# Performance work log

Measured on AMD Instinct MI355X. Metric: run time of the kernel, lower is better.

The kernel has to match this reference:

```python
import jax, jax.numpy as jnp
import numpy as np

B, N, H, FE, M, PASSES, OUT = 512, 40, 128, 16, 128, 3, 128
NEG = -1e9


def setup_inputs() -> dict:
    key = jax.random.key(0)
    ks = jax.random.split(key, 16)
    am = jax.random.bernoulli(ks[0], 0.1, (B, N, N))
    am = (am | jnp.swapaxes(am, 1, 2)) & (~jnp.eye(N, dtype=bool))[None]
    edges = jax.random.uniform(ks[1], (B, N, N, FE), dtype=jnp.float32) * am[..., None].astype(jnp.float32)
    nodes = jax.random.normal(ks[2], (B, N, H), dtype=jnp.float32)
    s = lambda f: 1.0 / np.sqrt(f)
    return {
        "nodes": nodes,
        "edges": edges,
        "We": jax.random.normal(ks[3], (FE, M), dtype=jnp.float32) * s(FE),
        "Wn": jax.random.normal(ks[4], (H, M), dtype=jnp.float32) * s(H),
        "Wm": jax.random.normal(ks[5], (H, M), dtype=jnp.float32) * s(H),
        "Wi": jax.random.normal(ks[6], (M, 3 * H), dtype=jnp.float32) * s(M),
        "Wh": jax.random.normal(ks[7], (H, 3 * H), dtype=jnp.float32) * s(H),
        "bi": jnp.zeros((3 * H,), jnp.float32),
        "bh": jnp.zeros((3 * H,), jnp.float32),
        "Wg": jax.random.normal(ks[8], (2 * H, OUT), dtype=jnp.float32) * s(2 * H),
        "bg": jnp.zeros((OUT,), jnp.float32),
        "Wo": jax.random.normal(ks[9], (2 * H, OUT), dtype=jnp.float32) * s(2 * H),
        "bo": jnp.zeros((OUT,), jnp.float32),
    }


def _forward(nodes, edges, We, Wn, Wm, Wi, Wh, bi, bh, Wg, bg, Wo, bo):
    adj = jnp.sum(edges, axis=3)                      # (B,N,N)
    nghb_mask = adj > 0                               # neighbor exists
    node_mask = jnp.any(nghb_mask, axis=-1)           # (B,N) node has >=1 neighbor

    h = nodes                                         # hidden == input feature dim
    edge_proj = jnp.einsum("bijf,fm->bijm", edges, We)  # precompute, edges fixed
    for _ in range(PASSES):
        # attention energies over neighbors j of node i (masked softmax)
        nghb_proj = jnp.einsum("bjh,hm->bjm", h, Wn)  # (B,N,M)
        e = jnp.tanh(edge_proj + nghb_proj[:, None, :, :])        # (B,N,N,M)
        e = jnp.where(nghb_mask[..., None], e, NEG)
        att = jax.nn.softmax(e, axis=2)                            # over neighbor axis j
        emb = jnp.einsum("bjh,hm->bjm", h, Wm)                     # (B,N,M)
        messages = jnp.einsum("bijm,bjm->bim", att, emb)           # (B,N,M)
        # GRU cell update (only for existing nodes, as in the node-batch scatter)
        gi = messages @ Wi + bi
        gh = h @ Wh + bh
        r = jax.nn.sigmoid(gi[..., :H] + gh[..., :H])
        z = jax.nn.sigmoid(gi[..., H:2 * H] + gh[..., H:2 * H])
        n = jnp.tanh(gi[..., 2 * H:] + r * gh[..., 2 * H:])
        h_new = (1.0 - z) * n + z * h
        h = jnp.where(node_mask[..., None], h_new, h)

    # gated graph readout over existing nodes
    cat = jnp.concatenate([h, nodes], axis=-1)        # (B,N,2H)
    gate = jax.nn.sigmoid(cat @ Wg + bg)
    emb_out = cat @ Wo + bo
    out = jnp.sum(node_mask[..., None] * gate * emb_out, axis=1)   # (B,OUT)
    return out


def reference(nodes, edges, We, Wn, Wm, Wi, Wh, bi, bh, Wg, bg, Wo, bo):
    return _forward(nodes, edges, We, Wn, Wm, Wi, Wh, bi, bh, Wg, bg, Wo, bo)
```

## Files before the change

### kernel.cpp

```cpp
#include <hip/hip_runtime.h>

#define T 512
constexpr int Bc = 512, Nc = 40, Hc = 128, FEc = 16, Mc = 128, OUTc = 128, NPASS = 3;
constexpr int ROWP = 136;
constexpr int NPP  = 132;
constexpr int EPOOL = 512;

typedef __attribute__((ext_vector_type(8))) short short8;
typedef __attribute__((ext_vector_type(4))) float floatx4;
typedef __attribute__((ext_vector_type(4))) float fvec4;
typedef _Float16 half2v __attribute__((ext_vector_type(2)));
typedef _Float16 half8v __attribute__((ext_vector_type(8)));

constexpr int WS_WN = 0, WS_WM = 16384, WS_WI = 32768, WS_WH = 81920, WS_WG = 131072, WS_WO = 163840;

__device__ __forceinline__ float fast_rcp(float x) { return __builtin_amdgcn_rcpf(x); }
__device__ __forceinline__ float fast_sigmoid(float x) { return fast_rcp(1.f + __expf(-x)); }
__device__ __forceinline__ float fast_tanh(float x) {
    float t = __expf(2.f * x);
    return 1.f - 2.f * fast_rcp(t + 1.f);
}
__device__ __forceinline__ float bf2f(unsigned short u) {
    union { unsigned int i; float f; } v; v.i = ((unsigned int)u) << 16; return v.f;
}
__device__ __forceinline__ unsigned short f2bf(float f) {
    union { float f; unsigned int i; } v; v.f = f;
    unsigned int r = v.i + 0x7fff + ((v.i >> 16) & 1);
    return (unsigned short)(r >> 16);
}
__device__ __forceinline__ half2v u2h(unsigned int u) {
    union { unsigned int i; half2v h; } v; v.i = u; return v.h;
}

__device__ __forceinline__ floatx4 mm(short8 a, short8 b, floatx4 c) {
    return __builtin_amdgcn_mfma_f32_16x16x32_bf16(a, b, c, 0, 0, 0);
}
__device__ __forceinline__ short8 afrag(const unsigned short* buf, int mt, int kt, int lane) {
    int row = mt * 16 + (lane & 15); row = row > 39 ? 39 : row;
    return *(const short8*)(buf + row * ROWP + kt * 32 + (lane >> 4) * 8);
}
__device__ __forceinline__ short8 bfrag(const unsigned short* w, int nt, int nKT, int kt, int lane) {
    return *(const short8*)(w + ((nt * nKT + kt) * 64 + lane) * 8);
}

__global__ void prep_kernel(const float* __restrict__ Wn, const float* __restrict__ Wm,
                            const float* __restrict__ Wi, const float* __restrict__ Wh,
                            const float* __restrict__ Wg, const float* __restrict__ Wo,
                            unsigned short* __restrict__ ws) {
    int c = blockIdx.x, lane = threadIdx.x;
    int quad = lane >> 4, l16 = lane & 15;
    const float* W; int N, nKT, local; unsigned short* dst;
    if (c < 32)       { W = Wn; N = 128; nKT = 4; local = c;       dst = ws + WS_WN; }
    else if (c < 64)  { W = Wm; N = 128; nKT = 4; local = c - 32;  dst = ws + WS_WM; }
    else if (c < 160) { W = Wi; N = 384; nKT = 4; local = c - 64;  dst = ws + WS_WI; }
    else if (c < 256) { W = Wh; N = 384; nKT = 4; local = c - 160; dst = ws + WS_WH; }
    else if (c < 320) { W = Wg; N = 128; nKT = 8; local = c - 256; dst = ws + WS_WG; }
    else              { W = Wo; N = 128; nKT = 8; local = c - 320; dst = ws + WS_WO; }
    int nt = local / nKT, kt = local % nKT;
    short8 v;
#pragma unroll
    for (int j = 0; j < 8; ++j) {
        int k = kt * 32 + quad * 8 + j;
        v[j] = (short)f2bf(W[k * N + nt * 16 + l16]);
    }
    *(short8*)(dst + local * 512 + lane * 8) = v;
}

__global__ __launch_bounds__(T, 4) void mpnn_kernel(
    const float* __restrict__ nodes, const float* __restrict__ edges,
    const float* __restrict__ We, const float* __restrict__ bi,
    const float* __restrict__ bh, const float* __restrict__ bg,
    const float* __restrict__ bo, const unsigned short* __restrict__ ws,
    float* __restrict__ out)
{
    __shared__ __attribute__((aligned(16))) unsigned short s_hb[Nc * ROWP];
    __shared__ __attribute__((aligned(16))) unsigned short s_mb[Nc * ROWP];
    __shared__ __attribute__((aligned(16))) float s_np[Nc * NPP];
    __shared__ __attribute__((aligned(16))) unsigned short s_eb[Nc * ROWP];
    __shared__ __attribute__((aligned(16))) _Float16 s_poolh[EPOOL * FEc];
    __shared__ unsigned char s_nbr[Nc][Nc];
    __shared__ int s_cnt[Nc];
    __shared__ int s_off[Nc];
    __shared__ int s_total;

    const int b = blockIdx.x, tid = threadIdx.x;
    const int lane = tid & 63, wave = tid >> 6;
    const int quad = lane >> 4, l16 = lane & 15;
    const int m = tid & 127, g = tid >> 7;
    const int col = wave * 16 + l16;

    const float* nodes_b = nodes + (size_t)b * Nc * Hc;
    const float* edges_b = edges + (size_t)b * Nc * Nc * FEc;
    const unsigned short* wWn = ws + WS_WN; const unsigned short* wWm = ws + WS_WM;
    const unsigned short* wWi = ws + WS_WI; const unsigned short* wWh = ws + WS_WH;
    const unsigned short* wWg = ws + WS_WG; const unsigned short* wWo = ws + WS_WO;

    float hreg[3][4];
#pragma unroll
    for (int mt = 0; mt < 3; ++mt)
#pragma unroll
        for (int reg = 0; reg < 4; ++reg) {
            int row = mt * 16 + quad * 4 + reg;
            float v = (row < Nc) ? nodes_b[row * Hc + col] : 0.f;
            hreg[mt][reg] = v;
            if (row < Nc) s_hb[row * ROWP + col] = f2bf(v);
        }
    for (int p = tid; p < Nc * Nc; p += T) {
        const fvec4* e4 = (const fvec4*)(edges_b + p * FEc);
        fvec4 a0 = __builtin_nontemporal_load(e4);
        fvec4 a1 = __builtin_nontemporal_load(e4 + 1);
        fvec4 a2 = __builtin_nontemporal_load(e4 + 2);
        fvec4 a3 = __builtin_nontemporal_load(e4 + 3);
        float s = a0.x + a0.y + a0.z + a0.w + a1.x + a1.y + a1.z + a1.w
                + a2.x + a2.y + a2.z + a2.w + a3.x + a3.y + a3.z + a3.w;
        ((unsigned char*)s_nbr)[p] = (s > 0.f) ? 1 : 0;
    }
    __syncthreads();
#pragma unroll 1
    for (int i = wave; i < Nc; i += 8) {
        unsigned char v = (lane < Nc) ? s_nbr[i][lane] : 0;
        unsigned long long mask = __ballot(v != 0);
        int rank = __popcll(mask & ((1ull << lane) - 1ull));
        if (v) s_nbr[i][rank] = (unsigned char)lane;
        if (lane == 0) s_cnt[i] = __popcll(mask);
    }
    __syncthreads();
    if (wave == 0) {
        int c = (lane < Nc) ? s_cnt[lane] : 0;
        int s = c;
#pragma unroll
        for (int d = 1; d < 64; d <<= 1) {
            int t = __shfl_up(s, d);
            if (lane >= d) s += t;
        }
        if (lane < Nc) s_off[lane] = s - c;
        if (lane == Nc - 1) s_total = s;
    }
    __syncthreads();
    int* slot_src = (int*)s_eb;
#pragma unroll 1
    for (int i = wave; i < Nc; i += 8) {
        int base = s_off[i], cnt = s_cnt[i];
        if (lane < cnt) {
            int slot = base + lane;
            if (slot < EPOOL) slot_src[slot] = i * Nc + s_nbr[i][lane];
        }
    }
    __syncthreads();
    {
        const int E = s_total < EPOOL ? s_total : EPOOL;
#pragma unroll 1
        for (int w = tid; w < E * 2; w += T) {
            int s = w >> 1, hf = w & 1;
            const float* src = edges_b + (size_t)slot_src[s] * FEc + hf * 8;
            fvec4 x = __builtin_nontemporal_load((const fvec4*)src);
            fvec4 y = __builtin_nontemporal_load((const fvec4*)(src + 4));
            half8v v;
            v[0] = (_Float16)x.x; v[1] = (_Float16)x.y; v[2] = (_Float16)x.z; v[3] = (_Float16)x.w;
            v[4] = (_Float16)y.x; v[5] = (_Float16)y.y; v[6] = (_Float16)y.z; v[7] = (_Float16)y.w;
            *(half8v*)(s_poolh + s * FEc + hf * 8) = v;
        }
    }
    __syncthreads();

    for (int pass = 0; pass < NPASS; ++pass) {
#pragma unroll 1
        for (int jb = 0; jb < 2; ++jb) {
            const unsigned short* wb = jb ? wWm : wWn;
            short8 bfr[4];
#pragma unroll
            for (int kt = 0; kt < 4; ++kt) bfr[kt] = bfrag(wb, wave, 4, kt, lane);
#pragma unroll 1
            for (int mt = 0; mt < 3; ++mt) {
                floatx4 acc = {0.f, 0.f, 0.f, 0.f};
#pragma unroll
                for (int kt = 0; kt < 4; ++kt) acc = mm(afrag(s_hb, mt, kt, lane), bfr[kt], acc);
#pragma unroll
                for (int reg = 0; reg < 4; ++reg) {
                    int row = mt * 16 + quad * 4 + reg;
                    if (row < Nc) {
                        if (jb) s_eb[row * ROWP + col] = f2bf(acc[reg]);
                        else    s_np[row * NPP + col] = acc[reg];
                    }
                }
            }
        }
        __syncthreads();

        {
#if __has_builtin(__builtin_amdgcn_fdot2)
            half2v wh[8];
#pragma unroll
            for (int f = 0; f < 8; ++f)
                wh[f] = (half2v){(_Float16)We[(2 * f) * Mc + m], (_Float16)We[(2 * f + 1) * Mc + m]};
#else
            float wef[FEc];
#pragma unroll
            for (int f = 0; f < FEc; ++f) wef[f] = We[f * Mc + m];
#endif
#pragma unroll 1
            for (int ib = 0; ib < 10; ++ib) {
                int i = g + ib * 4;
                int cnt = s_cnt[i], base = s_off[i];
                int cap = EPOOL - base; if (cap > cnt) cap = cnt; if (cap < 0) cap = 0;
                float pden = 0.f, pnum = 0.f;
                int kn = 0;
#pragma unroll 1
                for (; kn < cap; ++kn) {
                    int j = s_nbr[i][kn];
                    const uint4* e = (const uint4*)(s_poolh + (base + kn) * FEc);
                    uint4 p0 = e[0], p1 = e[1];
#if __has_builtin(__builtin_amdgcn_fdot2)
                    float ep = 0.f;
                    ep = __builtin_amdgcn_fdot2(u2h(p0.x), wh[0], ep, false);
                    ep = __builtin_amdgcn_fdot2(u2h(p0.y), wh[1], ep, false);
                    ep = __builtin_amdgcn_fdot2(u2h(p0.z), wh[2], ep, false);
                    ep = __builtin_amdgcn_fdot2(u2h(p0.w), wh[3], ep, false);
                    ep = __builtin_amdgcn_fdot2(u2h(p1.x), wh[4], ep, false);
                    ep = __builtin_amdgcn_fdot2(u2h(p1.y), wh[5], ep, false);
                    ep = __builtin_amdgcn_fdot2(u2h(p1.z), wh[6], ep, false);
                    ep = __builtin_amdgcn_fdot2(u2h(p1.w), wh[7], ep, false);
#else
                    half2v h0 = u2h(p0.x), h1 = u2h(p0.y), h2 = u2h(p0.z), h3 = u2h(p0.w);
                    half2v h4 = u2h(p1.x), h5 = u2h(p1.y), h6 = u2h(p1.z), h7 = u2h(p1.w);
                    float ep = (float)h0.x*wef[0] + (float)h0.y*wef[1] + (float)h1.x*wef[2] + (float)h1.y*wef[3]
                             + (float)h2.x*wef[4] + (float)h2.y*wef[5] + (float)h3.x*wef[6] + (float)h3.y*wef[7]
                             + (float)h4.x*wef[8] + (float)h4.y*wef[9] + (float)h5.x*wef[10]+ (float)h5.y*wef[11]
                             + (float)h6.x*wef[12]+ (float)h6.y*wef[13]+ (float)h7.x*wef[14]+ (float)h7.y*wef[15];
#endif
                    float x = ep + s_np[j * NPP + m];
                    float w = __expf(fast_tanh(x));
                    pden += w;
                    pnum += w * bf2f(s_eb[j * ROWP + m]);
                }
#pragma unroll 1
                for (; kn < cnt; ++kn) {
                    int j = s_nbr[i][kn];
                    const float4* ef = (const float4*)(edges_b + ((size_t)i * Nc + j) * FEc);
                    float4 a0 = ef[0], a1 = ef[1], a2 = ef[2], a3 = ef[3];
                    float ep = a0.x*We[0*Mc+m] + a0.y*We[1*Mc+m] + a0.z*We[2*Mc+m] + a0.w*We[3*Mc+m]
                             + a1.x*We[4*Mc+m] + a1.y*We[5*Mc+m] + a1.z*We[6*Mc+m] + a1.w*We[7*Mc+m]
                             + a2.x*We[8*Mc+m] + a2.y*We[9*Mc+m] + a2.z*We[10*Mc+m]+ a2.w*We[11*Mc+m]
                             + a3.x*We[12*Mc+m]+ a3.y*We[13*Mc+m]+ a3.z*We[14*Mc+m]+ a3.w*We[15*Mc+m];
                    float w = __expf(fast_tanh(ep + s_np[j * NPP + m]));
                    pden += w;
                    pnum += w * bf2f(s_eb[j * ROWP + m]);
                }
                s_mb[i * ROWP + m] = f2bf((cnt > 0) ? pnum * fast_rcp(pden) : 0.f);
            }
        }
        __syncthreads();

#pragma unroll 1
        for (int grp = 0; grp < 2; ++grp) {
            float bb = bi[grp * 128 + col] + bh[grp * 128 + col];
#pragma unroll 1
            for (int mt = 0; mt < 3; ++mt) {
                floatx4 acc = {0.f,0.f,0.f,0.f};
#pragma unroll 1
                for (int kt = 0; kt < 4; ++kt) {
                    acc = mm(afrag(s_mb, mt, kt, lane), bfrag(wWi, grp * 8 + wave, 4, kt, lane), acc);
                    acc = mm(afrag(s_hb, mt, kt, lane), bfrag(wWh, grp * 8 + wave, 4, kt, lane), acc);
                }
#pragma unroll
                for (int reg = 0; reg < 4; ++reg) {
                    int row = mt * 16 + quad * 4 + reg;
                    if (row < Nc) {
                        float sg = fast_sigmoid(acc[reg] + bb);
                        if (grp) s_eb[row * ROWP + col] = f2bf(sg);
                        else     s_np[row * NPP + col] = sg;
                    }
                }
            }
        }
        {
            float bnI = bi[256 + col], bnH = bh[256 + col];
#pragma unroll
            for (int mt = 0; mt < 3; ++mt) {
                floatx4 ai = {0.f,0.f,0.f,0.f}, ah = {0.f,0.f,0.f,0.f};
#pragma unroll 1
                for (int kt = 0; kt < 4; ++kt) {
                    ai = mm(afrag(s_mb, mt, kt, lane), bfrag(wWi, 16 + wave, 4, kt, lane), ai);
                    ah = mm(afrag(s_hb, mt, kt, lane), bfrag(wWh, 16 + wave, 4, kt, lane), ah);
                }
#pragma unroll
                for (int reg = 0; reg < 4; ++reg) {
                    int row = mt * 16 + quad * 4 + reg;
                    if (row < Nc) {
                        float hold = hreg[mt][reg];
                        float r = s_np[row * NPP + col];
                        float z = bf2f(s_eb[row * ROWP + col]);
                        float n = fast_tanh(ai[reg] + bnI + r * (ah[reg] + bnH));
                        float v = (1.f - z) * n + z * hold;
                        hreg[mt][reg] = (s_cnt[row] > 0) ? v : hold;
                    }
                }
            }
        }
        __syncthreads();
#pragma unroll
        for (int mt = 0; mt < 3; ++mt)
#pragma unroll
            for (int reg = 0; reg < 4; ++reg) {
                int row = mt * 16 + quad * 4 + reg;
                if (row < Nc) s_hb[row * ROWP + col] = f2bf(hreg[mt][reg]);
            }
        __syncthreads();
    }

    for (int idx = tid; idx < Nc * Hc; idx += T) {
        int row = idx >> 7, c2 = idx & 127;
        s_mb[row * ROWP + c2] = f2bf(nodes_b[idx]);
    }
    __syncthreads();
    float psum = 0.f;
    {
        float bgv = bg[col], bov = bo[col];
#pragma unroll 1
        for (int mt = 0; mt < 3; ++mt) {
            floatx4 ga = {0.f,0.f,0.f,0.f}, oa = {0.f,0.f,0.f,0.f};
#pragma unroll 1
            for (int kt = 0; kt < 8; ++kt) {
                short8 a = (kt < 4) ? afrag(s_hb, mt, kt, lane) : afrag(s_mb, mt, kt - 4, lane);
                ga = mm(a, bfrag(wWg, wave, 8, kt, lane), ga);
                oa = mm(a, bfrag(wWo, wave, 8, kt, lane), oa);
            }
#pragma unroll
            for (int reg = 0; reg < 4; ++reg) {
                int row = mt * 16 + quad * 4 + reg;
                if (row < Nc && s_cnt[row] > 0)
                    psum += fast_sigmoid(ga[reg] + bgv) * (oa[reg] + bov);
            }
        }
    }
    psum += __shfl_xor(psum, 16);
    psum += __shfl_xor(psum, 32);
    if (quad == 0) out[(size_t)b * OUTc + col] = psum;
}

extern "C" void kernel_launch(void* const* d_in, const int* in_sizes, int n_in,
                              void* d_out, int out_size, void* d_ws, size_t ws_size,
                              hipStream_t stream) {
    const float* nodes = (const float*)d_in[0];
    const float* edges = (const float*)d_in[1];
    const float* We = (const float*)d_in[2];
    const float* Wn = (const float*)d_in[3];
    const float* Wm = (const float*)d_in[4];
    const float* Wi = (const float*)d_in[5];
    const float* Wh = (const float*)d_in[6];
    const float* bi = (const float*)d_in[7];
    const float* bh = (const float*)d_in[8];
    const float* Wg = (const float*)d_in[9];
    const float* bg = (const float*)d_in[10];
    const float* Wo = (const float*)d_in[11];
    const float* bo = (const float*)d_in[12];
    float* out = (float*)d_out;
    unsigned short* ws = (unsigned short*)d_ws;

    prep_kernel<<<384, 64, 0, stream>>>(Wn, Wm, Wi, Wh, Wg, Wo, ws);
    mpnn_kernel<<<Bc, T, 0, stream>>>(nodes, edges, We, bi, bh, bg, bo, ws, out);
}
```

Baseline: 248.4 us.

## Double block size to 1024 threads and split GEMM phases across wave halves

Raises the block to 16 waves and divides the work between two wave halves. One half computes the Wn projection while the other computes Wm, and the r and z gate GEMMs are split the same way. The attention loop now covers 8 node groups instead of 4. The candidate-gate update and readout run on only the lower half, which needs an extra barrier and leaves half the waves idle in those phases. The launch-bounds change to (1024, 8) may raise register pressure and lower how many blocks fit per CU, given the large LDS footprint.

```diff
diff --git a/kernel.cpp b/kernel.cpp
--- a/kernel.cpp
+++ b/kernel.cpp
@@ -1,6 +1,6 @@
 #include <hip/hip_runtime.h>
 
-#define T 512
+#define T 1024
 constexpr int Bc = 512, Nc = 40, Hc = 128, FEc = 16, Mc = 128, OUTc = 128, NPASS = 3;
 constexpr int ROWP = 136;
 constexpr int NPP  = 132;
@@ -66,7 +66,7 @@
     *(short8*)(dst + local * 512 + lane * 8) = v;
 }
 
-__global__ __launch_bounds__(T, 4) void mpnn_kernel(
+__global__ __launch_bounds__(T, 8) void mpnn_kernel(
     const float* __restrict__ nodes, const float* __restrict__ edges,
     const float* __restrict__ We, const float* __restrict__ bi,
     const float* __restrict__ bh, const float* __restrict__ bg,
@@ -86,8 +86,9 @@
     const int b = blockIdx.x, tid = threadIdx.x;
     const int lane = tid & 63, wave = tid >> 6;
     const int quad = lane >> 4, l16 = lane & 15;
+    const int hi = wave >> 3, nt8 = wave & 7;
     const int m = tid & 127, g = tid >> 7;
-    const int col = wave * 16 + l16;
+    const int col = nt8 * 16 + l16;
 
     const float* nodes_b = nodes + (size_t)b * Nc * Hc;
     const float* edges_b = edges + (size_t)b * Nc * Nc * FEc;
@@ -96,15 +97,17 @@
     const unsigned short* wWg = ws + WS_WG; const unsigned short* wWo = ws + WS_WO;
 
     float hreg[3][4];
-#pragma unroll
-    for (int mt = 0; mt < 3; ++mt)
-#pragma unroll
-        for (int reg = 0; reg < 4; ++reg) {
-            int row = mt * 16 + quad * 4 + reg;
-            float v = (row < Nc) ? nodes_b[row * Hc + col] : 0.f;
-            hreg[mt][reg] = v;
-            if (row < Nc) s_hb[row * ROWP + col] = f2bf(v);
-        }
+    if (hi == 0) {
+#pragma unroll
+        for (int mt = 0; mt < 3; ++mt)
+#pragma unroll
+            for (int reg = 0; reg < 4; ++reg) {
+                int row = mt * 16 + quad * 4 + reg;
+                float v = (row < Nc) ? nodes_b[row * Hc + col] : 0.f;
+                hreg[mt][reg] = v;
+                if (row < Nc) s_hb[row * ROWP + col] = f2bf(v);
+            }
+    }
     for (int p = tid; p < Nc * Nc; p += T) {
         const fvec4* e4 = (const fvec4*)(edges_b + p * FEc);
         fvec4 a0 = __builtin_nontemporal_load(e4);
@@ -117,7 +120,7 @@
     }
     __syncthreads();
 #pragma unroll 1
-    for (int i = wave; i < Nc; i += 8) {
+    for (int i = wave; i < Nc; i += 16) {
         unsigned char v = (lane < Nc) ? s_nbr[i][lane] : 0;
         unsigned long long mask = __ballot(v != 0);
         int rank = __popcll(mask & ((1ull << lane) - 1ull));
@@ -139,7 +142,7 @@
     __syncthreads();
     int* slot_src = (int*)s_eb;
 #pragma unroll 1
-    for (int i = wave; i < Nc; i += 8) {
+    for (int i = wave; i < Nc; i += 16) {
         int base = s_off[i], cnt = s_cnt[i];
         if (lane < cnt) {
             int slot = base + lane;
@@ -164,12 +167,11 @@
     __syncthreads();
 
     for (int pass = 0; pass < NPASS; ++pass) {
-#pragma unroll 1
-        for (int jb = 0; jb < 2; ++jb) {
-            const unsigned short* wb = jb ? wWm : wWn;
+        {
+            const unsigned short* wb = hi ? wWm : wWn;
             short8 bfr[4];
 #pragma unroll
-            for (int kt = 0; kt < 4; ++kt) bfr[kt] = bfrag(wb, wave, 4, kt, lane);
+            for (int kt = 0; kt < 4; ++kt) bfr[kt] = bfrag(wb, nt8, 4, kt, lane);
 #pragma unroll 1
             for (int mt = 0; mt < 3; ++mt) {
                 floatx4 acc = {0.f, 0.f, 0.f, 0.f};
@@ -179,7 +181,7 @@
                 for (int reg = 0; reg < 4; ++reg) {
                     int row = mt * 16 + quad * 4 + reg;
                     if (row < Nc) {
-                        if (jb) s_eb[row * ROWP + col] = f2bf(acc[reg]);
+                        if (hi) s_eb[row * ROWP + col] = f2bf(acc[reg]);
                         else    s_np[row * NPP + col] = acc[reg];
                     }
                 }
@@ -199,8 +201,8 @@
             for (int f = 0; f < FEc; ++f) wef[f] = We[f * Mc + m];
 #endif
 #pragma unroll 1
-            for (int ib = 0; ib < 10; ++ib) {
-                int i = g + ib * 4;
+            for (int ib = 0; ib < 5; ++ib) {
+                int i = g + ib * 8;
                 int cnt = s_cnt[i], base = s_off[i];
                 int cap = EPOOL - base; if (cap > cnt) cap = cnt; if (cap < 0) cap = 0;
                 float pden = 0.f, pnum = 0.f;
@@ -251,16 +253,16 @@
         }
         __syncthreads();
 
-#pragma unroll 1
-        for (int grp = 0; grp < 2; ++grp) {
+        {
+            const int grp = hi;
             float bb = bi[grp * 128 + col] + bh[grp * 128 + col];
 #pragma unroll 1
             for (int mt = 0; mt < 3; ++mt) {
                 floatx4 acc = {0.f,0.f,0.f,0.f};
 #pragma unroll 1
                 for (int kt = 0; kt < 4; ++kt) {
-                    acc = mm(afrag(s_mb, mt, kt, lane), bfrag(wWi, grp * 8 + wave, 4, kt, lane), acc);
-                    acc = mm(afrag(s_hb, mt, kt, lane), bfrag(wWh, grp * 8 + wave, 4, kt, lane), acc);
+                    acc = mm(afrag(s_mb, mt, kt, lane), bfrag(wWi, grp * 8 + nt8, 4, kt, lane), acc);
+                    acc = mm(afrag(s_hb, mt, kt, lane), bfrag(wWh, grp * 8 + nt8, 4, kt, lane), acc);
                 }
 #pragma unroll
                 for (int reg = 0; reg < 4; ++reg) {
@@ -273,15 +275,17 @@
                 }
             }
         }
-        {
+        __syncthreads();
+
+        if (hi == 0) {
             float bnI = bi[256 + col], bnH = bh[256 + col];
 #pragma unroll
             for (int mt = 0; mt < 3; ++mt) {
                 floatx4 ai = {0.f,0.f,0.f,0.f}, ah = {0.f,0.f,0.f,0.f};
 #pragma unroll 1
                 for (int kt = 0; kt < 4; ++kt) {
-                    ai = mm(afrag(s_mb, mt, kt, lane), bfrag(wWi, 16 + wave, 4, kt, lane), ai);
-                    ah = mm(afrag(s_hb, mt, kt, lane), bfrag(wWh, 16 + wave, 4, kt, lane), ah);
+                    ai = mm(afrag(s_mb, mt, kt, lane), bfrag(wWi, 16 + nt8, 4, kt, lane), ai);
+                    ah = mm(afrag(s_hb, mt, kt, lane), bfrag(wWh, 16 + nt8, 4, kt, lane), ah);
                 }
 #pragma unroll
                 for (int reg = 0; reg < 4; ++reg) {
@@ -298,13 +302,15 @@
             }
         }
         __syncthreads();
-#pragma unroll
-        for (int mt = 0; mt < 3; ++mt)
-#pragma unroll
-            for (int reg = 0; reg < 4; ++reg) {
-                int row = mt * 16 + quad * 4 + reg;
-                if (row < Nc) s_hb[row * ROWP + col] = f2bf(hreg[mt][reg]);
-            }
+        if (hi == 0) {
+#pragma unroll
+            for (int mt = 0; mt < 3; ++mt)
+#pragma unroll
+                for (int reg = 0; reg < 4; ++reg) {
+                    int row = mt * 16 + quad * 4 + reg;
+                    if (row < Nc) s_hb[row * ROWP + col] = f2bf(hreg[mt][reg]);
+                }
+        }
         __syncthreads();
     }
 
@@ -313,29 +319,31 @@
         s_mb[row * ROWP + c2] = f2bf(nodes_b[idx]);
     }
     __syncthreads();
-    float psum = 0.f;
-    {
-        float bgv = bg[col], bov = bo[col];
-#pragma unroll 1
-        for (int mt = 0; mt < 3; ++mt) {
-            floatx4 ga = {0.f,0.f,0.f,0.f}, oa = {0.f,0.f,0.f,0.f};
-#pragma unroll 1
-            for (int kt = 0; kt < 8; ++kt) {
-                short8 a = (kt < 4) ? afrag(s_hb, mt, kt, lane) : afrag(s_mb, mt, kt - 4, lane);
-                ga = mm(a, bfrag(wWg, wave, 8, kt, lane), ga);
-                oa = mm(a, bfrag(wWo, wave, 8, kt, lane), oa);
-            }
-#pragma unroll
-            for (int reg = 0; reg < 4; ++reg) {
-                int row = mt * 16 + quad * 4 + reg;
-                if (row < Nc && s_cnt[row] > 0)
-                    psum += fast_sigmoid(ga[reg] + bgv) * (oa[reg] + bov);
-            }
-        }
-    }
-    psum += __shfl_xor(psum, 16);
-    psum += __shfl_xor(psum, 32);
-    if (quad == 0) out[(size_t)b * OUTc + col] = psum;
+    if (hi == 0) {
+        float psum = 0.f;
+        {
+            float bgv = bg[col], bov = bo[col];
+#pragma unroll 1
+            for (int mt = 0; mt < 3; ++mt) {
+                floatx4 ga = {0.f,0.f,0.f,0.f}, oa = {0.f,0.f,0.f,0.f};
+#pragma unroll 1
+                for (int kt = 0; kt < 8; ++kt) {
+                    short8 a = (kt < 4) ? afrag(s_hb, mt, kt, lane) : afrag(s_mb, mt, kt - 4, lane);
+                    ga = mm(a, bfrag(wWg, nt8, 8, kt, lane), ga);
+                    oa = mm(a, bfrag(wWo, nt8, 8, kt, lane), oa);
+                }
+#pragma unroll
+                for (int reg = 0; reg < 4; ++reg) {
+                    int row = mt * 16 + quad * 4 + reg;
+                    if (row < Nc && s_cnt[row] > 0)
+                        psum += fast_sigmoid(ga[reg] + bgv) * (oa[reg] + bov);
+                }
+            }
+        }
+        psum += __shfl_xor(psum, 16);
+        psum += __shfl_xor(psum, 32);
+        if (quad == 0) out[(size_t)b * OUTc + col] = psum;
+    }
 }
 
 extern "C" void kernel_launch(void* const* d_in, const int* in_sizes, int n_in,
```

Measured after the change: 333.8 us. 34.4% more time.
